# Kernel optimization log

Hardware: AMD Instinct MI355X
Metric: run time of the kernel (lower is better)

The kernel has to match this reference:

```python
import jax, jax.numpy as jnp
import numpy as np

D_MODEL = 1024
N_HEADS = 16
HEAD_DIM = D_MODEL // N_HEADS
ROPE_BASE = 10000.0


def rotate_half(x):
    d = x.shape[-1]
    x1, x2 = x[..., : d // 2], x[..., d // 2 :]
    return jnp.concatenate((-x2, x1), axis=-1)


def rope_cos_sin(T, dim, dtype):
    inv_freq = 1.0 / (ROPE_BASE ** (jnp.arange(0, dim, 2, dtype=jnp.float32) / dim))
    t = jnp.arange(T, dtype=jnp.float32)
    freqs = jnp.einsum('i,j->ij', t, inv_freq)  # (T, dim//2)
    emb = jnp.concatenate((freqs, freqs), axis=-1)  # (T, dim)
    return jnp.cos(emb).astype(dtype), jnp.sin(emb).astype(dtype)


def setup_inputs() -> dict:
    key = jax.random.key(0)
    ks = jax.random.split(key, 9)
    s = 0.02
    return {
        'x': jax.random.normal(ks[0], (4, 2048, D_MODEL), dtype=jnp.float32),
        'Wq': jax.random.normal(ks[1], (D_MODEL, D_MODEL), dtype=jnp.float32) * s,
        'bq': jax.random.normal(ks[2], (D_MODEL,), dtype=jnp.float32) * s,
        'Wk': jax.random.normal(ks[3], (D_MODEL, D_MODEL), dtype=jnp.float32) * s,
        'bk': jax.random.normal(ks[4], (D_MODEL,), dtype=jnp.float32) * s,
        'Wv': jax.random.normal(ks[5], (D_MODEL, D_MODEL), dtype=jnp.float32) * s,
        'bv': jax.random.normal(ks[6], (D_MODEL,), dtype=jnp.float32) * s,
        'Wo': jax.random.normal(ks[7], (D_MODEL, D_MODEL), dtype=jnp.float32) * s,
        'bo': jax.random.normal(ks[8], (D_MODEL,), dtype=jnp.float32) * s,
    }


def reference(x, Wq, bq, Wk, bk, Wv, bv, Wo, bo):
    B, T, D = x.shape
    H, hd = N_HEADS, HEAD_DIM

    def proj(W, b):
        y = jnp.einsum('btd,ed->bte', x, W) + b  # torch Linear: x @ W.T + b
        return y.reshape(B, T, H, hd).transpose(0, 2, 1, 3)  # (B,H,T,hd)

    q = proj(Wq, bq)
    k = proj(Wk, bk)
    v = proj(Wv, bv)

    cos, sin = rope_cos_sin(T, hd, x.dtype)  # (T, hd)
    q = q * cos + rotate_half(q) * sin
    k = k * cos + rotate_half(k) * sin

    scores = jnp.einsum('bhqd,bhkd->bhqk', q, k) / jnp.sqrt(jnp.asarray(hd, x.dtype))
    causal = jnp.tril(jnp.ones((T, T), dtype=bool))
    scores = jnp.where(causal, scores, jnp.asarray(-jnp.inf, x.dtype))
    attn = jax.nn.softmax(scores, axis=-1)  # dropout=0 (eval)
    out = jnp.einsum('bhqk,bhkd->bhqd', attn, v)
    out = out.transpose(0, 2, 1, 3).reshape(B, T, D)
    return jnp.einsum('btd,ed->bte', out, Wo) + bo
```

## Files before the change

### kernel.cpp

```cpp
#include <hip/hip_runtime.h>
#include <math.h>

typedef unsigned short u16;
typedef unsigned int u32;
typedef __attribute__((ext_vector_type(4))) float f32x4;
typedef __attribute__((ext_vector_type(8))) __bf16 bf16x8;
typedef __attribute__((ext_vector_type(2))) __bf16 bf16x2;
typedef __attribute__((ext_vector_type(2))) u32 u32x2;

#define B_ 4
#define T_ 2048
#define D_ 1024
#define H_ 16
#define HD_ 64

__device__ __forceinline__ u16 f2b_rne(float f) {
  u32 u = __float_as_uint(f);
  u32 r = (u + 0x7FFFu + ((u >> 16) & 1u)) >> 16;
  return (u16)r;
}
__device__ __forceinline__ float b2f(u16 u) {
  return __uint_as_float(((u32)u) << 16);
}
__device__ __forceinline__ u32 pack2(float a, float b) {
  bf16x2 v = {(__bf16)a, (__bf16)b};
  return __builtin_bit_cast(u32, v);
}
__device__ __forceinline__ void gload_lds16(const void* g, void* l) {
  __builtin_amdgcn_global_load_lds(
      (const __attribute__((address_space(1))) u32*)g,
      (__attribute__((address_space(3))) u32*)l, 16, 0, 0);
}

__global__ void f2b4_kernel(const float* __restrict__ in, u16* __restrict__ out, int n4) {
  int i = blockIdx.x * 256 + threadIdx.x;
  if (i < n4) {
    f32x4 v = ((const f32x4*)in)[i];
    u32x2 o;
    o.x = pack2(v[0], v[1]);
    o.y = pack2(v[2], v[3]);
    ((u32x2*)out)[i] = o;
  }
}

__global__ void f2bw_kernel(const float* __restrict__ Wq, const float* __restrict__ Wk,
                            const float* __restrict__ Wv, const float* __restrict__ Wo,
                            u16* __restrict__ wqkv, u16* __restrict__ wo) {
  int sel = blockIdx.x >> 10;
  int i = (blockIdx.x & 1023) * 256 + threadIdx.x;
  const float* src = sel == 0 ? Wq : sel == 1 ? Wk : sel == 2 ? Wv : Wo;
  u16* dst = sel < 3 ? wqkv + (size_t)sel * (D_ * D_) : wo;
  f32x4 v = ((const f32x4*)src)[i];
  u32x2 o;
  o.x = pack2(v[0], v[1]);
  o.y = pack2(v[2], v[3]);
  ((u32x2*)dst)[i] = o;
}

__global__ void rope_qk_kernel(const u16* __restrict__ qkv,
                               u16* __restrict__ Q, u16* __restrict__ K) {
  int j = blockIdx.x * 256 + threadIdx.x;
  if (j >= (B_ * T_) * (D_ / 2)) return;
  int row = j >> 9;
  int p = j & 511;
  int h = p >> 5, i = p & 31;
  int b = row >> 11, t = row & (T_ - 1);
  const u16* base = qkv + (size_t)row * (3 * D_);
  float inv_freq = exp2f(-(float)i * 0.4152410118609203f);
  float ang = (float)t * inv_freq;
  float s, c;
  sincosf(ang, &s, &c);
  int qi = h * HD_ + i;
  float q1 = b2f(base[qi]),      q2 = b2f(base[qi + 32]);
  float k1 = b2f(base[D_ + qi]), k2 = b2f(base[D_ + qi + 32]);
  const float QS = 0.18033688011f;
  float qo1 = (q1 * c - q2 * s) * QS;
  float qo2 = (q2 * c + q1 * s) * QS;
  float ko1 = k1 * c - k2 * s;
  float ko2 = k2 * c + k1 * s;
  size_t bh = (size_t)(b * H_ + h);
  size_t qk = bh * T_ * HD_ + (size_t)t * HD_ + i;
  Q[qk]      = f2b_rne(qo1);
  Q[qk + 32] = f2b_rne(qo2);
  K[qk]      = f2b_rne(ko1);
  K[qk + 32] = f2b_rne(ko2);
}

__global__ __launch_bounds__(256) void vt_kernel(const u16* __restrict__ qkv,
                                                 u16* __restrict__ VT) {
  __shared__ __align__(16) u16 tile[64 * 64];
  const int x = blockIdx.x;
  const int bh = blockIdx.y;
  const int b = bh >> 4, h = bh & 15;
  const int tid = threadIdx.x;
  const u16* src = qkv + (size_t)(b * T_ + x * 64) * (3 * D_) + 2 * D_ + h * HD_;
#pragma unroll
  for (int it = 0; it < 2; ++it) {
    int r = it * 32 + (tid >> 3);
    int chunk = tid & 7;
    bf16x8 v = *(const bf16x8*)(src + (size_t)r * (3 * D_) + chunk * 8);
    u16 tmp[8];
    *(bf16x8*)tmp = v;
#pragma unroll
    for (int jj = 0; jj < 8; ++jj) {
      int i = chunk * 8 + jj;
      int byte = i * 128 + ((2 * r) ^ ((i >> 3) << 4));
      *(u16*)((char*)tile + byte) = tmp[jj];
    }
  }
  __syncthreads();
  const int i = tid >> 2, tc = tid & 3;
  u16* dst = VT + (size_t)bh * HD_ * T_ + (size_t)i * T_ + x * 64 + tc * 16;
#pragma unroll
  for (int half = 0; half < 2; ++half) {
    int byte = i * 128 + ((tc * 32 + half * 16) ^ ((i >> 3) << 4));
    *(bf16x8*)(dst + half * 8) = *(const bf16x8*)((char*)tile + byte);
  }
}

template <bool F32OUT>
__global__ __launch_bounds__(256) void gemm_bt_kernel(
    const u16* __restrict__ A, const u16* __restrict__ Bm,
    const float* __restrict__ bias, void* __restrict__ Cout,
    int M, int N, int K) {
  __shared__ __align__(16) u16 As[128 * 64];
  __shared__ __align__(16) u16 Bs[128 * 64];
  const int tid = threadIdx.x;
  const int wid = tid >> 6, lane = tid & 63;
  const int l15 = lane & 15, lhi = lane >> 4;
  const int NY = gridDim.y;
  int lin = blockIdx.y * 64 + blockIdx.x;
  int qq = (NY << 6) >> 3;
  int swz = (lin & 7) * qq + (lin >> 3);
  const int brow = swz / NY;
  const int bcol = swz - brow * NY;
  const int wr = wid >> 1, wc = wid & 1;

  f32x4 acc[4][4] = {};

  for (int k0 = 0; k0 < K; k0 += 64) {
#pragma unroll
    for (int cc = 0; cc < 4; cc++) {
      int chunk = cc * 4 + wid;
      int slot = chunk * 64 + lane;
      int row = slot >> 3;
      int colb = (slot & 7) << 4;
      gload_lds16((const char*)(A + (size_t)(brow * 128 + row) * K + k0) + colb,
                  (char*)As + chunk * 1024);
      gload_lds16((const char*)(Bm + (size_t)(bcol * 128 + row) * K + k0) + colb,
                  (char*)Bs + chunk * 1024);
    }
    __syncthreads();
#pragma unroll
    for (int kk = 0; kk < 2; kk++) {
      bf16x8 af[4], bfr[4];
#pragma unroll
      for (int i = 0; i < 4; i++)
        af[i] = *(const bf16x8*)&As[(wr * 64 + i * 16 + l15) * 64 + kk * 32 + lhi * 8];
#pragma unroll
      for (int j = 0; j < 4; j++)
        bfr[j] = *(const bf16x8*)&Bs[(wc * 64 + j * 16 + l15) * 64 + kk * 32 + lhi * 8];
#pragma unroll
      for (int i = 0; i < 4; i++)
#pragma unroll
        for (int j = 0; j < 4; j++)
          acc[i][j] = __builtin_amdgcn_mfma_f32_16x16x32_bf16(af[i], bfr[j], acc[i][j], 0, 0, 0);
    }
    __syncthreads();
  }
#pragma unroll
  for (int i = 0; i < 4; i++)
#pragma unroll
    for (int r = 0; r < 4; r++) {
      int row = brow * 128 + wr * 64 + i * 16 + lhi * 4 + r;
#pragma unroll
      for (int j = 0; j < 4; j++) {
        int col = bcol * 128 + wc * 64 + j * 16 + l15;
        float v = acc[i][j][r] + bias[col];
        if (F32OUT)
          ((float*)Cout)[(size_t)row * N + col] = v;
        else
          ((u16*)Cout)[(size_t)row * N + col] = f2b_rne(v);
      }
    }
}

__global__ __launch_bounds__(256) void attn_kernel(
    const u16* __restrict__ Q, const u16* __restrict__ K,
    const u16* __restrict__ VT, u16* __restrict__ O) {
  __shared__ __align__(16) u16 Plds[4][2][16 * 64];
  const int tid = threadIdx.x;
  const int w = tid >> 6, lane = tid & 63;
  const int l15 = lane & 15, lhi = lane >> 4;
  const int xcd = blockIdx.x & 7;
  const int j = blockIdx.x >> 3;
  const int bh = (xcd << 3) | (j & 7);
  const int a = ((j >> 3) << 2) | w;
  const int kt = a >> 2;
  const int bb = bh >> 4, hh = bh & 15;

  const u16* Qb = Q + (size_t)bh * T_ * HD_;
  const u16* Kb = K + (size_t)bh * T_ * HD_;
  const u16* Vb = VT + (size_t)bh * HD_ * T_;
  const int sw = (l15 & 7) << 4;
  const float CMAX = 16.f;

  const int qrw[2] = {a * 16 + l15, (127 - a) * 16 + l15};

  bf16x8 qf[2][2];
#pragma unroll
  for (int g = 0; g < 2; ++g) {
    const u16* qr = Qb + (size_t)qrw[g] * HD_ + lhi * 8;
    qf[g][0] = *(const bf16x8*)(qr);
    qf[g][1] = *(const bf16x8*)(qr + 32);
  }

  float lp[2] = {0.f, 0.f};
  f32x4 oacc[2][4] = {};

  auto smpv = [&](int g, f32x4* sg, bf16x8 vf[4][2]) {
    char* prow = (char*)&Plds[w][g][0] + l15 * 128;
    float rsp = 0.f;
#pragma unroll
    for (int ks = 0; ks < 4; ++ks) {
      float e0 = exp2f(sg[ks][0] - CMAX);
      float e1 = exp2f(sg[ks][1] - CMAX);
      float e2 = exp2f(sg[ks][2] - CMAX);
      float e3 = exp2f(sg[ks][3] - CMAX);
      rsp += (e0 + e1) + (e2 + e3);
      u32x2 pw;
      pw.x = pack2(e0, e1);
      pw.y = pack2(e2, e3);
      *(u32x2*)(prow + ((ks * 32 + lhi * 8) ^ sw)) = pw;
    }
    lp[g] += rsp;
#pragma unroll
    for (int c = 0; c < 2; ++c) {
      bf16x8 pb = *(const bf16x8*)((const char*)prow + ((c * 64 + lhi * 16) ^ sw));
#pragma unroll
      for (int db = 0; db < 4; ++db)
        oacc[g][db] = __builtin_amdgcn_mfma_f32_16x16x32_bf16(vf[db][c], pb, oacc[g][db], 0, 0, 0);
    }
  };
  auto maskdiag = [&](int g, f32x4* sg, int t0) {
#pragma unroll
    for (int ks = 0; ks < 4; ++ks)
#pragma unroll
      for (int r = 0; r < 4; ++r)
        if (t0 + ks * 16 + lhi * 4 + r > qrw[g]) sg[ks][r] = -1e30f;
  };
  auto loadV = [&](int t0, bf16x8 vf[4][2]) {
#pragma unroll
    for (int db = 0; db < 4; ++db) {
      const u16* vr = Vb + (size_t)(db * 16 + l15) * T_ + t0 + lhi * 8;
      vf[db][0] = *(const bf16x8*)(vr);
      vf[db][1] = *(const bf16x8*)(vr + 32);
    }
  };

  for (int t = 0; t <= kt; ++t) {
    const int t0 = t * 64;
    f32x4 s[2][4];
#pragma unroll
    for (int ks = 0; ks < 4; ++ks) {
      const u16* kr = Kb + (size_t)(t0 + ks * 16 + l15) * HD_ + lhi * 8;
      bf16x8 kf0 = *(const bf16x8*)(kr);
      bf16x8 kf1 = *(const bf16x8*)(kr + 32);
#pragma unroll
      for (int g = 0; g < 2; ++g) {
        f32x4 z = {0.f, 0.f, 0.f, 0.f};
        z = __builtin_amdgcn_mfma_f32_16x16x32_bf16(kf0, qf[g][0], z, 0, 0, 0);
        s[g][ks] = __builtin_amdgcn_mfma_f32_16x16x32_bf16(kf1, qf[g][1], z, 0, 0, 0);
      }
    }
    bf16x8 vf[4][2];
    loadV(t0, vf);
    if (t == kt) maskdiag(0, s[0], t0);
    smpv(0, s[0], vf);
    smpv(1, s[1], vf);
  }

  for (int t = kt + 1; t <= 31 - kt; ++t) {
    const int t0 = t * 64;
    f32x4 s1[4];
#pragma unroll
    for (int ks = 0; ks < 4; ++ks) {
      const u16* kr = Kb + (size_t)(t0 + ks * 16 + l15) * HD_ + lhi * 8;
      bf16x8 kf0 = *(const bf16x8*)(kr);
      bf16x8 kf1 = *(const bf16x8*)(kr + 32);
      f32x4 z = {0.f, 0.f, 0.f, 0.f};
      z = __builtin_amdgcn_mfma_f32_16x16x32_bf16(kf0, qf[1][0], z, 0, 0, 0);
      s1[ks] = __builtin_amdgcn_mfma_f32_16x16x32_bf16(kf1, qf[1][1], z, 0, 0, 0);
    }
    bf16x8 vf[4][2];
    loadV(t0, vf);
    if (t == 31 - kt) maskdiag(1, s1, t0);
    smpv(1, s1, vf);
  }

#pragma unroll
  for (int g = 0; g < 2; ++g) {
    float l = lp[g];
    l += __shfl_xor(l, 16);
    l += __shfl_xor(l, 32);
    float invl = 1.0f / l;
    u16* orow = O + ((size_t)bb * T_ + qrw[g]) * D_ + hh * HD_ + lhi * 4;
#pragma unroll
    for (int db = 0; db < 4; ++db) {
      u32x2 wv;
      wv.x = pack2(oacc[g][db][0] * invl, oacc[g][db][1] * invl);
      wv.y = pack2(oacc[g][db][2] * invl, oacc[g][db][3] * invl);
      *(u32x2*)(orow + db * 16) = wv;
    }
  }
}

extern "C" void kernel_launch(void* const* d_in, const int* in_sizes, int n_in,
                              void* d_out, int out_size, void* d_ws, size_t ws_size,
                              hipStream_t stream) {
  const float* x  = (const float*)d_in[0];
  const float* Wq = (const float*)d_in[1];
  const float* bq = (const float*)d_in[2];
  const float* Wk = (const float*)d_in[3];
  const float* bk = (const float*)d_in[4];
  const float* Wv = (const float*)d_in[5];
  const float* bv = (const float*)d_in[6];
  const float* Wo = (const float*)d_in[7];
  const float* bo = (const float*)d_in[8];

  char* ws = (char*)d_ws;
  u16*  XB    = (u16*)(ws + 0);
  u16*  QKV   = (u16*)(ws + 16777216);
  u16*  Qb    = (u16*)(ws + 67108864);
  u16*  Kb    = (u16*)(ws + 83886080);
  u16*  VTb   = (u16*)(ws + 100663296);
  u16*  WQKVB = (u16*)(ws + 117440512);
  u16*  WOB   = (u16*)(ws + 123731968);
  float* BQKV = (float*)(ws + 125829120);
  u16*  ATTO  = XB;

  hipMemcpyAsync(BQKV,        bq, D_ * 4, hipMemcpyDeviceToDevice, stream);
  hipMemcpyAsync(BQKV + D_,   bk, D_ * 4, hipMemcpyDeviceToDevice, stream);
  hipMemcpyAsync(BQKV + 2*D_, bv, D_ * 4, hipMemcpyDeviceToDevice, stream);

  f2b4_kernel<<<8192, 256, 0, stream>>>(x, XB, B_ * T_ * D_ / 4);
  f2bw_kernel<<<4096, 256, 0, stream>>>(Wq, Wk, Wv, Wo, WQKVB, WOB);

  gemm_bt_kernel<false><<<dim3(64, 24), 256, 0, stream>>>(
      XB, WQKVB, BQKV, QKV, B_ * T_, 3 * D_, D_);

  rope_qk_kernel<<<16384, 256, 0, stream>>>(QKV, Qb, Kb);
  vt_kernel<<<dim3(T_ / 64, B_ * H_), 256, 0, stream>>>(QKV, VTb);

  attn_kernel<<<1024, 256, 0, stream>>>(Qb, Kb, VTb, ATTO);

  gemm_bt_kernel<true><<<dim3(64, 8), 256, 0, stream>>>(
      ATTO, WOB, bo, d_out, B_ * T_, D_, D_);

  (void)in_sizes; (void)n_in; (void)out_size; (void)ws_size;
}
```

Before: 336.2 us.

## Double-buffer K/V register tiles and merge the two attention loops

Restructures the causal attention loop into a single loop that prefetches the next K and V tiles into a second register buffer while computing on the current one, unrolled by two to ping-pong the buffers. The separate diagonal and tail loops are merged into one body that branches on whether both query groups are active. It also reorders softmax and PV so the two groups' work interleaves. This aims to hide global load latency behind MFMA work, at the cost of more VGPRs, which may reduce occupancy or cause spills.

```diff
diff --git a/kernel.cpp b/kernel.cpp
--- a/kernel.cpp
+++ b/kernel.cpp
@@ -197,6 +197,7 @@
   const int bh = (xcd << 3) | (j & 7);
   const int a = ((j >> 3) << 2) | w;
   const int kt = a >> 2;
+  const int tEnd = 31 - kt;
   const int bb = bh >> 4, hh = bh & 15;
 
   const u16* Qb = Q + (size_t)bh * T_ * HD_;
@@ -218,7 +219,38 @@
   float lp[2] = {0.f, 0.f};
   f32x4 oacc[2][4] = {};
 
-  auto smpv = [&](int g, f32x4* sg, bf16x8 vf[4][2]) {
+  auto loadK = [&](int t0, bf16x8* kf) {
+#pragma unroll
+    for (int ks = 0; ks < 4; ++ks) {
+      const u16* kr = Kb + (size_t)(t0 + ks * 16 + l15) * HD_ + lhi * 8;
+      kf[ks * 2]     = *(const bf16x8*)(kr);
+      kf[ks * 2 + 1] = *(const bf16x8*)(kr + 32);
+    }
+  };
+  auto loadV = [&](int t0, bf16x8* vf) {
+#pragma unroll
+    for (int db = 0; db < 4; ++db) {
+      const u16* vr = Vb + (size_t)(db * 16 + l15) * T_ + t0 + lhi * 8;
+      vf[db * 2]     = *(const bf16x8*)(vr);
+      vf[db * 2 + 1] = *(const bf16x8*)(vr + 32);
+    }
+  };
+  auto qk = [&](const bf16x8* kf, int g, f32x4* sg) {
+#pragma unroll
+    for (int ks = 0; ks < 4; ++ks) {
+      f32x4 z = {0.f, 0.f, 0.f, 0.f};
+      z = __builtin_amdgcn_mfma_f32_16x16x32_bf16(kf[ks * 2], qf[g][0], z, 0, 0, 0);
+      sg[ks] = __builtin_amdgcn_mfma_f32_16x16x32_bf16(kf[ks * 2 + 1], qf[g][1], z, 0, 0, 0);
+    }
+  };
+  auto maskdiag = [&](int g, f32x4* sg, int t0) {
+#pragma unroll
+    for (int ks = 0; ks < 4; ++ks)
+#pragma unroll
+      for (int r = 0; r < 4; ++r)
+        if (t0 + ks * 16 + lhi * 4 + r > qrw[g]) sg[ks][r] = -1e30f;
+  };
+  auto sm = [&](int g, f32x4* sg) {
     char* prow = (char*)&Plds[w][g][0] + l15 * 128;
     float rsp = 0.f;
 #pragma unroll
@@ -234,68 +266,48 @@
       *(u32x2*)(prow + ((ks * 32 + lhi * 8) ^ sw)) = pw;
     }
     lp[g] += rsp;
+  };
+  auto pv = [&](int g, const bf16x8* vf) {
+    const char* prow = (const char*)&Plds[w][g][0] + l15 * 128;
 #pragma unroll
     for (int c = 0; c < 2; ++c) {
-      bf16x8 pb = *(const bf16x8*)((const char*)prow + ((c * 64 + lhi * 16) ^ sw));
+      bf16x8 pb = *(const bf16x8*)(prow + ((c * 64 + lhi * 16) ^ sw));
 #pragma unroll
       for (int db = 0; db < 4; ++db)
-        oacc[g][db] = __builtin_amdgcn_mfma_f32_16x16x32_bf16(vf[db][c], pb, oacc[g][db], 0, 0, 0);
-    }
-  };
-  auto maskdiag = [&](int g, f32x4* sg, int t0) {
-#pragma unroll
-    for (int ks = 0; ks < 4; ++ks)
-#pragma unroll
-      for (int r = 0; r < 4; ++r)
-        if (t0 + ks * 16 + lhi * 4 + r > qrw[g]) sg[ks][r] = -1e30f;
-  };
-  auto loadV = [&](int t0, bf16x8 vf[4][2]) {
-#pragma unroll
-    for (int db = 0; db < 4; ++db) {
-      const u16* vr = Vb + (size_t)(db * 16 + l15) * T_ + t0 + lhi * 8;
-      vf[db][0] = *(const bf16x8*)(vr);
-      vf[db][1] = *(const bf16x8*)(vr + 32);
-    }
-  };
-
-  for (int t = 0; t <= kt; ++t) {
+        oacc[g][db] = __builtin_amdgcn_mfma_f32_16x16x32_bf16(vf[db * 2 + c], pb, oacc[g][db], 0, 0, 0);
+    }
+  };
+  auto body = [&](int t, const bf16x8* kf, const bf16x8* vf) {
     const int t0 = t * 64;
-    f32x4 s[2][4];
-#pragma unroll
-    for (int ks = 0; ks < 4; ++ks) {
-      const u16* kr = Kb + (size_t)(t0 + ks * 16 + l15) * HD_ + lhi * 8;
-      bf16x8 kf0 = *(const bf16x8*)(kr);
-      bf16x8 kf1 = *(const bf16x8*)(kr + 32);
-#pragma unroll
-      for (int g = 0; g < 2; ++g) {
-        f32x4 z = {0.f, 0.f, 0.f, 0.f};
-        z = __builtin_amdgcn_mfma_f32_16x16x32_bf16(kf0, qf[g][0], z, 0, 0, 0);
-        s[g][ks] = __builtin_amdgcn_mfma_f32_16x16x32_bf16(kf1, qf[g][1], z, 0, 0, 0);
-      }
-    }
-    bf16x8 vf[4][2];
-    loadV(t0, vf);
-    if (t == kt) maskdiag(0, s[0], t0);
-    smpv(0, s[0], vf);
-    smpv(1, s[1], vf);
-  }
-
-  for (int t = kt + 1; t <= 31 - kt; ++t) {
-    const int t0 = t * 64;
+    const bool both = (t <= kt);
     f32x4 s1[4];
-#pragma unroll
-    for (int ks = 0; ks < 4; ++ks) {
-      const u16* kr = Kb + (size_t)(t0 + ks * 16 + l15) * HD_ + lhi * 8;
-      bf16x8 kf0 = *(const bf16x8*)(kr);
-      bf16x8 kf1 = *(const bf16x8*)(kr + 32);
-      f32x4 z = {0.f, 0.f, 0.f, 0.f};
-      z = __builtin_amdgcn_mfma_f32_16x16x32_bf16(kf0, qf[1][0], z, 0, 0, 0);
-      s1[ks] = __builtin_amdgcn_mfma_f32_16x16x32_bf16(kf1, qf[1][1], z, 0, 0, 0);
-    }
-    bf16x8 vf[4][2];
-    loadV(t0, vf);
-    if (t == 31 - kt) maskdiag(1, s1, t0);
-    smpv(1, s1, vf);
+    qk(kf, 1, s1);
+    if (t == tEnd) maskdiag(1, s1, t0);
+    if (both) {
+      f32x4 s0[4];
+      qk(kf, 0, s0);
+      if (t == kt) maskdiag(0, s0, t0);
+      sm(1, s1);
+      sm(0, s0);
+      pv(1, vf);
+      pv(0, vf);
+    } else {
+      sm(1, s1);
+      pv(1, vf);
+    }
+  };
+
+  bf16x8 kA[8], vA[8], kB[8], vB[8];
+  loadK(0, kA);
+  loadV(0, vA);
+  int t = 0;
+  for (;;) {
+    if (t < tEnd) { loadK((t + 1) * 64, kB); loadV((t + 1) * 64, vB); }
+    body(t, kA, vA);
+    if (++t > tEnd) break;
+    if (t < tEnd) { loadK((t + 1) * 64, kA); loadV((t + 1) * 64, vA); }
+    body(t, kB, vB);
+    if (++t > tEnd) break;
   }
 
 #pragma unroll
```

Result: no change. 336.0 us (-0.1%).
